# Optimization experiments

Measured on AMD Instinct MI355X. Metric: run time of the kernel, lower is better.

The kernel has to match this reference:

```python
import jax, jax.numpy as jnp
import numpy as np

V = 50000
E = 640000
DIM = 128
NUM_EDGE_TYPES = 32


def setup_inputs() -> dict:
    key = jax.random.key(0)
    ks = jax.random.split(key, 8)
    return {
        "node_values": jax.random.normal(ks[0], (V, DIM), dtype=jnp.float32),
        "edge_src": jax.random.randint(ks[1], (E,), 0, V, dtype=jnp.int32),
        "edge_dest": jax.random.randint(ks[2], (E,), 0, V, dtype=jnp.int32),
        "edge_cls": jax.random.randint(ks[3], (E,), 0, NUM_EDGE_TYPES, dtype=jnp.int32),
        "W_src": jax.random.normal(ks[4], (DIM, DIM), dtype=jnp.float32) / np.sqrt(DIM),
        "b_src": jnp.zeros((DIM,), dtype=jnp.float32),
        "W_dest": jax.random.normal(ks[5], (DIM, DIM), dtype=jnp.float32) / np.sqrt(DIM),
        "b_dest": jnp.zeros((DIM,), dtype=jnp.float32),
        "edge_emb": jax.random.normal(ks[6], (NUM_EDGE_TYPES, DIM), dtype=jnp.float32),
    }


def reference(node_values, edge_src, edge_dest, edge_cls, W_src, b_src, W_dest, b_dest, edge_emb):
    # Dense projections over all nodes, then gather per edge (matches tf.gather(dense(...), idx))
    src_proj = node_values @ W_src + b_src    # [V, dim]
    dest_proj = node_values @ W_dest + b_dest  # [V, dim]
    # Per-edge fused message: gather src, gather dest, edge-class embedding lookup, add, relu
    msgs = jax.nn.relu(src_proj[edge_src] + dest_proj[edge_dest] + edge_emb[edge_cls])  # [E, dim]
    # Scatter-reduce messages onto destination nodes
    out = jax.ops.segment_sum(msgs, edge_dest, num_segments=V)  # [V, dim]
    return out
```

## Files before the change

### kernel.cpp

```cpp
#include <hip/hip_runtime.h>


#define V 50000
#define E 640000
#define DIM 128
#define NXCD 8
#define DRANGE 6250
#define NBIN_R 50
#define BINW 125
#define BINCAP 2048
#define NCHUNK 256
#define EC4 625
#define QCAP 384

typedef __bf16 bf16x8 __attribute__((ext_vector_type(8)));
typedef float  f32x4  __attribute__((ext_vector_type(4)));
typedef float  f32x2  __attribute__((ext_vector_type(2)));

__device__ __forceinline__ float bf2f(unsigned int u16) {
    union { unsigned int i; float f; } c; c.i = u16 << 16; return c.f;
}
__device__ __forceinline__ unsigned int f2bf(float f) {
    union { float f; unsigned int i; } c; c.f = f;
    unsigned int u = c.i;
    return (u + 0x7FFFu + ((u >> 16) & 1u)) >> 16;
}

__global__ __launch_bounds__(256) void mp_binA(
    const int* __restrict__ ed, const int* __restrict__ es, const int* __restrict__ ec,
    const float* __restrict__ Ws, const float* __restrict__ Wd,
    const float* __restrict__ emb,
    unsigned short* __restrict__ Wpk, unsigned short* __restrict__ embB,
    int* __restrict__ binCnt, int* __restrict__ binbuf)
{
    __shared__ int hist[4][NBIN_R];
    __shared__ int cur[NBIN_R];
    const int r = blockIdx.x & (NXCD - 1);
    const int c = blockIdx.x >> 3;
    const int dlo = r * DRANGE;
    const int t = threadIdx.x;
    const int wv = t >> 6;

    if (blockIdx.x < 16) {
        int tid = blockIdx.x * 256 + t;
        int mat  = tid >> 11;
        int rem  = tid & 2047;
        int ct   = rem >> 8;
        int kt   = (rem >> 6) & 3;
        int lane = rem & 63;
        const float* W = mat ? Wd : Ws;
        int n  = ct * 16 + (lane & 15);
        int k0 = kt * 32 + (lane >> 4) * 8;
        unsigned short* dst = Wpk + (size_t)tid * 8;
        #pragma unroll
        for (int j = 0; j < 8; ++j) dst[j] = (unsigned short)f2bf(W[(k0 + j) * DIM + n]);
        embB[tid] = (unsigned short)f2bf(emb[tid]);
    }

    if (t < 4 * NBIN_R) ((int*)hist)[t] = 0;
    __syncthreads();

    int4 DV[3], SV[3], CV[3];
    {
        const int4* ed4 = (const int4*)ed + c * EC4;
        const int4* es4 = (const int4*)es + c * EC4;
        const int4* ec4 = (const int4*)ec + c * EC4;
        #pragma unroll
        for (int k = 0; k < 3; ++k) {
            int i = t + k * 256;
            if (i < EC4) { DV[k] = ed4[i]; SV[k] = es4[i]; CV[k] = ec4[i]; }
            else { DV[k] = make_int4(-1, -1, -1, -1);
                   SV[k] = make_int4(0, 0, 0, 0); CV[k] = make_int4(0, 0, 0, 0); }
        }
    }

    #pragma unroll
    for (int k = 0; k < 3; ++k) {
        int rel;
        rel = DV[k].x - dlo; if ((unsigned)rel < DRANGE) atomicAdd(&hist[wv][(unsigned)rel / BINW], 1);
        rel = DV[k].y - dlo; if ((unsigned)rel < DRANGE) atomicAdd(&hist[wv][(unsigned)rel / BINW], 1);
        rel = DV[k].z - dlo; if ((unsigned)rel < DRANGE) atomicAdd(&hist[wv][(unsigned)rel / BINW], 1);
        rel = DV[k].w - dlo; if ((unsigned)rel < DRANGE) atomicAdd(&hist[wv][(unsigned)rel / BINW], 1);
    }
    __syncthreads();

    if (t < NBIN_R) {
        int h = hist[0][t] + hist[1][t] + hist[2][t] + hist[3][t];
        cur[t] = atomicAdd(&binCnt[r * NBIN_R + t], h);
    }
    __syncthreads();

    #pragma unroll
    for (int k = 0; k < 3; ++k) {
        #define TRY(D, S, C) { \
            int rel = (D) - dlo; \
            if ((unsigned)rel < DRANGE) { \
                int bin = (unsigned)rel / BINW; \
                int rl  = rel - bin * BINW; \
                int pos = atomicAdd(&cur[bin], 1); \
                if ((unsigned)pos < BINCAP) \
                    binbuf[(r * NBIN_R + bin) * BINCAP + pos] = \
                        ((S) & 0xFFFF) | ((C) << 16) | (rl << 21); \
            } }
        TRY(DV[k].x, SV[k].x, CV[k].x); TRY(DV[k].y, SV[k].y, CV[k].y);
        TRY(DV[k].z, SV[k].z, CV[k].z); TRY(DV[k].w, SV[k].w, CV[k].w);
        #undef TRY
    }
}

__global__ __launch_bounds__(256) void mp_proj(
    const float* __restrict__ x, const unsigned short* __restrict__ Wpk,
    const float* __restrict__ bs, const float* __restrict__ bd,
    unsigned char* __restrict__ ps8, unsigned short* __restrict__ pdB)
{
    __shared__ float stage[4][16 * 132];
    const int wave = __builtin_amdgcn_readfirstlane(threadIdx.x) >> 6;
    const int lane = threadIdx.x & 63;
    const int m = lane & 15, q = lane >> 4;
    const int row0 = blockIdx.x * 64 + wave * 16;

    int arow = row0 + m; if (arow >= V) arow = V - 1;
    const float* xr = x + (size_t)arow * DIM + q * 8;

    bf16x8 A[4];
    #pragma unroll
    for (int kt = 0; kt < 4; ++kt) {
        float4 u = *(const float4*)(xr + kt * 32);
        float4 v = *(const float4*)(xr + kt * 32 + 4);
        bf16x8 a;
        a[0] = (__bf16)u.x; a[1] = (__bf16)u.y; a[2] = (__bf16)u.z; a[3] = (__bf16)u.w;
        a[4] = (__bf16)v.x; a[5] = (__bf16)v.y; a[6] = (__bf16)v.z; a[7] = (__bf16)v.w;
        A[kt] = a;
    }

    const bf16x8* Bp = (const bf16x8*)Wpk;

    f32x4 accS[8], accD[8];
    #pragma unroll
    for (int ct = 0; ct < 8; ++ct) {
        f32x4 aS = {0.f, 0.f, 0.f, 0.f}, aD = {0.f, 0.f, 0.f, 0.f};
        #pragma unroll
        for (int kt = 0; kt < 4; ++kt) {
            bf16x8 bS = Bp[((0 * 8 + ct) * 4 + kt) * 64 + lane];
            bf16x8 bD = Bp[((1 * 8 + ct) * 4 + kt) * 64 + lane];
            aS = __builtin_amdgcn_mfma_f32_16x16x32_bf16(A[kt], bS, aS, 0, 0, 0);
            aD = __builtin_amdgcn_mfma_f32_16x16x32_bf16(A[kt], bD, aD, 0, 0, 0);
        }
        accS[ct] = aS; accD[ct] = aD;
    }

    float* st = stage[wave];
    const int rr = lane & 15, cg = lane >> 4;
    const int orow = row0 + rr;
    const float* rowp = st + rr * 132 + cg * 32;

    #pragma unroll
    for (int ct = 0; ct < 8; ++ct) {
        const float bv = bs[ct * 16 + m];
        #pragma unroll
        for (int r = 0; r < 4; ++r)
            st[(q * 4 + r) * 132 + ct * 16 + m] = accS[ct][r] + bv;
    }
    __syncthreads();
    {
        int w[8];
        #pragma unroll
        for (int j = 0; j < 8; ++j) {
            float4 f = *(const float4*)(rowp + 4 * j);
            int v = __builtin_amdgcn_cvt_pk_fp8_f32(f.x, f.y, 0, false);
            v = __builtin_amdgcn_cvt_pk_fp8_f32(f.z, f.w, v, true);
            w[j] = v;
        }
        if (orow < V) {
            int4* dst = (int4*)(ps8 + (size_t)orow * 128 + cg * 32);
            dst[0] = make_int4(w[0], w[1], w[2], w[3]);
            dst[1] = make_int4(w[4], w[5], w[6], w[7]);
        }
    }
    __syncthreads();

    #pragma unroll
    for (int ct = 0; ct < 8; ++ct) {
        const float bv = bd[ct * 16 + m];
        #pragma unroll
        for (int r = 0; r < 4; ++r)
            st[(q * 4 + r) * 132 + ct * 16 + m] = accD[ct][r] + bv;
    }
    __syncthreads();
    {
        int w[16];
        #pragma unroll
        for (int j = 0; j < 8; ++j) {
            float4 f = *(const float4*)(rowp + 4 * j);
            w[2 * j]     = f2bf(f.x) | (f2bf(f.y) << 16);
            w[2 * j + 1] = f2bf(f.z) | (f2bf(f.w) << 16);
        }
        if (orow < V) {
            int4* dst = (int4*)(pdB + (size_t)orow * 128 + cg * 32);
            #pragma unroll
            for (int jj = 0; jj < 4; ++jj)
                dst[jj] = make_int4(w[4 * jj], w[4 * jj + 1], w[4 * jj + 2], w[4 * jj + 3]);
        }
    }
}

__global__ __launch_bounds__(256) void mp_binBC(
    const unsigned char* __restrict__ ps8, const unsigned short* __restrict__ pdB,
    const unsigned short* __restrict__ embB,
    const int* __restrict__ binCnt, const int* __restrict__ binbuf,
    float* __restrict__ out)
{
    __shared__ int csr[QCAP];
    __shared__ int cnt[16];
    __shared__ int off[17];
    __shared__ int cur[16];

    const int r = blockIdx.x & (NXCD - 1);
    const int rest = blockIdx.x >> 3;
    const int bi = rest % NBIN_R;
    const int qu = rest / NBIN_R;
    const int bin = r * NBIN_R + bi;
    const int rel0 = qu * 16;
    const int relW = (qu == 7) ? 13 : 16;
    const int d0 = bin * BINW + rel0;
    const int t = threadIdx.x;

    int nb = binCnt[bin]; if (nb > BINCAP) nb = BINCAP;
    const int* buf = binbuf + (size_t)bin * BINCAP;

    if (t < 16) cnt[t] = 0;
    __syncthreads();

    int EB[8];
    #pragma unroll
    for (int k = 0; k < 8; ++k) {
        int i = t + k * 256;
        EB[k] = (i < nb) ? buf[i] : -1;
    }

    #pragma unroll
    for (int k = 0; k < 8; ++k) {
        int rl = (int)((unsigned)EB[k] >> 21) - rel0;
        if ((unsigned)rl < (unsigned)relW) atomicAdd(&cnt[rl], 1);
    }
    __syncthreads();

    if (t < 16) {
        int v = (t < relW) ? cnt[t] : 0;
        #pragma unroll
        for (int dlt = 1; dlt < 16; dlt <<= 1) {
            int u = __shfl_up(v, dlt, 64);
            if (t >= dlt) v += u;
        }
        off[t + 1] = v;
        cur[t] = v - cnt[t];
        if (t == 0) off[0] = 0;
    }
    __syncthreads();

    #pragma unroll
    for (int k = 0; k < 8; ++k) {
        int rl = (int)((unsigned)EB[k] >> 21) - rel0;
        if ((unsigned)rl < (unsigned)relW) {
            int pos = atomicAdd(&cur[rl], 1);
            if (pos < QCAP) csr[pos] = EB[k];
        }
    }
    __syncthreads();

    const int wave = t >> 6, lane = t & 63;
    #define PROC(P) { \
        int s_ = *(const unsigned short*)(ps8 + ((size_t)((P) & 0xFFFF) << 7) + 2 * lane); \
        unsigned int e_ = *(const unsigned int*)(embB + ((((P) >> 16) & 0x1F) << 7) + 2 * lane); \
        f32x2 f_ = __builtin_amdgcn_cvt_pk_f32_fp8(s_, false); \
        a0 += fmaxf(f_.x + dp0 + bf2f(e_ & 0xFFFF), 0.f); \
        a1 += fmaxf(f_.y + dp1 + bf2f(e_ >> 16),    0.f); }

    for (int rl = wave; rl < relW; rl += 4) {
        const int d = d0 + rl;
        int i0 = off[rl], i1 = off[rl + 1];
        if (i1 > QCAP) i1 = QCAP;
        if (i0 > i1) i0 = i1;
        unsigned int pdu = *(const unsigned int*)(pdB + (size_t)d * DIM + 2 * lane);
        const float dp0 = bf2f(pdu & 0xFFFF), dp1 = bf2f(pdu >> 16);
        float a0 = 0.f, a1 = 0.f;
        int i = i0;
        for (; i + 8 <= i1; i += 8) {
            int p0 = csr[i],     p1 = csr[i + 1], p2 = csr[i + 2], p3 = csr[i + 3];
            int p4 = csr[i + 4], p5 = csr[i + 5], p6 = csr[i + 6], p7 = csr[i + 7];
            PROC(p0); PROC(p1); PROC(p2); PROC(p3);
            PROC(p4); PROC(p5); PROC(p6); PROC(p7);
        }
        for (; i + 4 <= i1; i += 4) {
            int p0 = csr[i], p1 = csr[i + 1], p2 = csr[i + 2], p3 = csr[i + 3];
            PROC(p0); PROC(p1); PROC(p2); PROC(p3);
        }
        for (; i < i1; ++i) { int p0 = csr[i]; PROC(p0); }
        *(float2*)(out + (size_t)d * DIM + 2 * lane) = make_float2(a0, a1);
    }
    #undef PROC
}

extern "C" void kernel_launch(void* const* d_in, const int* in_sizes, int n_in,
                              void* d_out, int out_size, void* d_ws, size_t ws_size,
                              hipStream_t stream) {
    const float* x   = (const float*)d_in[0];
    const int*   es  = (const int*)d_in[1];
    const int*   ed  = (const int*)d_in[2];
    const int*   ec  = (const int*)d_in[3];
    const float* Ws  = (const float*)d_in[4];
    const float* bs  = (const float*)d_in[5];
    const float* Wd  = (const float*)d_in[6];
    const float* bd  = (const float*)d_in[7];
    const float* emb = (const float*)d_in[8];
    float* out = (float*)d_out;

    char* ws = (char*)d_ws;
    size_t off = 0;
    unsigned char*  ps8  = (unsigned char*)(ws + off);  off += (size_t)V * 128;
    unsigned short* pdB  = (unsigned short*)(ws + off); off += (size_t)V * DIM * 2;
    int* binbuf = (int*)(ws + off);                     off += (size_t)400 * BINCAP * 4;
    int* binCnt = (int*)(ws + off);                     off += 400 * 4;
    unsigned short* Wpk  = (unsigned short*)(ws + off); off += 2 * 128 * 128 * 2;
    unsigned short* embB = (unsigned short*)(ws + off); off += 32 * 128 * 2;

    hipMemsetAsync(binCnt, 0, 400 * 4, stream);
    mp_binA<<<NXCD * NCHUNK, 256, 0, stream>>>(ed, es, ec, Ws, Wd, emb, Wpk, embB, binCnt, binbuf);
    mp_proj<<<(V + 63) / 64, 256, 0, stream>>>(x, Wpk, bs, bd, ps8, pdB);
    mp_binBC<<<NBIN_R * NXCD * 8, 256, 0, stream>>>(ps8, pdB, embB, binCnt, binbuf, out);
}
```

Baseline: 154.7 us.

## Use 16-node bins so each consumer block reads only its own bin

Changes the destination binning from 50 bins of 125 nodes per XCD to 391 bins of 16 nodes, using shift and mask in place of division. Each consumer block now loads only its own small bin (up to 320 entries) instead of scanning a 2048-entry bin and discarding seven eighths of it, which removes redundant global reads and filtering. The destination projection rows are also prefetched before the first barrier. The cost is a larger shared histogram and more global bin counters and atomics in the binning kernel, and the per-bin capacity of 320 could overflow on skewed inputs.

```diff
diff --git a/kernel.cpp b/kernel.cpp
--- a/kernel.cpp
+++ b/kernel.cpp
@@ -6,12 +6,10 @@
 #define DIM 128
 #define NXCD 8
 #define DRANGE 6250
-#define NBIN_R 50
-#define BINW 125
-#define BINCAP 2048
+#define NBIN_R 391
+#define BINCAP 320
 #define NCHUNK 256
 #define EC4 625
-#define QCAP 384
 
 typedef __bf16 bf16x8 __attribute__((ext_vector_type(8)));
 typedef float  f32x4  __attribute__((ext_vector_type(4)));
@@ -57,7 +55,7 @@
         embB[tid] = (unsigned short)f2bf(emb[tid]);
     }
 
-    if (t < 4 * NBIN_R) ((int*)hist)[t] = 0;
+    for (int i = t; i < 4 * NBIN_R; i += 256) ((int*)hist)[i] = 0;
     __syncthreads();
 
     int4 DV[3], SV[3], CV[3];
@@ -77,16 +75,16 @@
     #pragma unroll
     for (int k = 0; k < 3; ++k) {
         int rel;
-        rel = DV[k].x - dlo; if ((unsigned)rel < DRANGE) atomicAdd(&hist[wv][(unsigned)rel / BINW], 1);
-        rel = DV[k].y - dlo; if ((unsigned)rel < DRANGE) atomicAdd(&hist[wv][(unsigned)rel / BINW], 1);
-        rel = DV[k].z - dlo; if ((unsigned)rel < DRANGE) atomicAdd(&hist[wv][(unsigned)rel / BINW], 1);
-        rel = DV[k].w - dlo; if ((unsigned)rel < DRANGE) atomicAdd(&hist[wv][(unsigned)rel / BINW], 1);
-    }
-    __syncthreads();
-
-    if (t < NBIN_R) {
-        int h = hist[0][t] + hist[1][t] + hist[2][t] + hist[3][t];
-        cur[t] = atomicAdd(&binCnt[r * NBIN_R + t], h);
+        rel = DV[k].x - dlo; if ((unsigned)rel < DRANGE) atomicAdd(&hist[wv][(unsigned)rel >> 4], 1);
+        rel = DV[k].y - dlo; if ((unsigned)rel < DRANGE) atomicAdd(&hist[wv][(unsigned)rel >> 4], 1);
+        rel = DV[k].z - dlo; if ((unsigned)rel < DRANGE) atomicAdd(&hist[wv][(unsigned)rel >> 4], 1);
+        rel = DV[k].w - dlo; if ((unsigned)rel < DRANGE) atomicAdd(&hist[wv][(unsigned)rel >> 4], 1);
+    }
+    __syncthreads();
+
+    for (int i = t; i < NBIN_R; i += 256) {
+        int h = hist[0][i] + hist[1][i] + hist[2][i] + hist[3][i];
+        cur[i] = atomicAdd(&binCnt[r * NBIN_R + i], h);
     }
     __syncthreads();
 
@@ -95,8 +93,8 @@
         #define TRY(D, S, C) { \
             int rel = (D) - dlo; \
             if ((unsigned)rel < DRANGE) { \
-                int bin = (unsigned)rel / BINW; \
-                int rl  = rel - bin * BINW; \
+                int bin = (unsigned)rel >> 4; \
+                int rl  = rel & 15; \
                 int pos = atomicAdd(&cur[bin], 1); \
                 if ((unsigned)pos < BINCAP) \
                     binbuf[(r * NBIN_R + bin) * BINCAP + pos] = \
@@ -210,38 +208,43 @@
     const int* __restrict__ binCnt, const int* __restrict__ binbuf,
     float* __restrict__ out)
 {
-    __shared__ int csr[QCAP];
+    __shared__ int csr[BINCAP];
     __shared__ int cnt[16];
     __shared__ int off[17];
     __shared__ int cur[16];
 
     const int r = blockIdx.x & (NXCD - 1);
-    const int rest = blockIdx.x >> 3;
-    const int bi = rest % NBIN_R;
-    const int qu = rest / NBIN_R;
-    const int bin = r * NBIN_R + bi;
-    const int rel0 = qu * 16;
-    const int relW = (qu == 7) ? 13 : 16;
-    const int d0 = bin * BINW + rel0;
+    const int g = blockIdx.x >> 3;
+    const int bin = r * NBIN_R + g;
+    const int rel0 = g * 16;
+    const int relW = (rel0 + 16 <= DRANGE) ? 16 : (DRANGE - rel0);
+    const int d0 = r * DRANGE + rel0;
     const int t = threadIdx.x;
+    const int wave = t >> 6, lane = t & 63;
 
     int nb = binCnt[bin]; if (nb > BINCAP) nb = BINCAP;
     const int* buf = binbuf + (size_t)bin * BINCAP;
 
     if (t < 16) cnt[t] = 0;
-    __syncthreads();
-
-    int EB[8];
-    #pragma unroll
-    for (int k = 0; k < 8; ++k) {
-        int i = t + k * 256;
-        EB[k] = (i < nb) ? buf[i] : -1;
-    }
-
-    #pragma unroll
-    for (int k = 0; k < 8; ++k) {
-        int rl = (int)((unsigned)EB[k] >> 21) - rel0;
-        if ((unsigned)rl < (unsigned)relW) atomicAdd(&cnt[rl], 1);
+
+    int EB[2];
+    EB[0] = (t < nb) ? buf[t] : -1;
+    EB[1] = (t + 256 < nb) ? buf[t + 256] : -1;
+
+    float dp0v[4], dp1v[4];
+    #pragma unroll
+    for (int k = 0; k < 4; ++k) {
+        int rl = wave + k * 4;
+        int d = d0 + ((rl < relW) ? rl : 0);
+        unsigned int pdu = *(const unsigned int*)(pdB + (size_t)d * DIM + 2 * lane);
+        dp0v[k] = bf2f(pdu & 0xFFFF); dp1v[k] = bf2f(pdu >> 16);
+    }
+    __syncthreads();
+
+    #pragma unroll
+    for (int k = 0; k < 2; ++k) {
+        int rl = (int)((unsigned)EB[k] >> 21);
+        if (EB[k] != -1) atomicAdd(&cnt[rl], 1);
     }
     __syncthreads();
 
@@ -259,16 +262,15 @@
     __syncthreads();
 
     #pragma unroll
-    for (int k = 0; k < 8; ++k) {
-        int rl = (int)((unsigned)EB[k] >> 21) - rel0;
-        if ((unsigned)rl < (unsigned)relW) {
+    for (int k = 0; k < 2; ++k) {
+        if (EB[k] != -1) {
+            int rl = (int)((unsigned)EB[k] >> 21);
             int pos = atomicAdd(&cur[rl], 1);
-            if (pos < QCAP) csr[pos] = EB[k];
-        }
-    }
-    __syncthreads();
-
-    const int wave = t >> 6, lane = t & 63;
+            csr[pos] = EB[k];
+        }
+    }
+    __syncthreads();
+
     #define PROC(P) { \
         int s_ = *(const unsigned short*)(ps8 + ((size_t)((P) & 0xFFFF) << 7) + 2 * lane); \
         unsigned int e_ = *(const unsigned int*)(embB + ((((P) >> 16) & 0x1F) << 7) + 2 * lane); \
@@ -276,13 +278,13 @@
         a0 += fmaxf(f_.x + dp0 + bf2f(e_ & 0xFFFF), 0.f); \
         a1 += fmaxf(f_.y + dp1 + bf2f(e_ >> 16),    0.f); }
 
-    for (int rl = wave; rl < relW; rl += 4) {
+    #pragma unroll
+    for (int k = 0; k < 4; ++k) {
+        const int rl = wave + k * 4;
+        if (rl >= relW) break;
         const int d = d0 + rl;
         int i0 = off[rl], i1 = off[rl + 1];
-        if (i1 > QCAP) i1 = QCAP;
-        if (i0 > i1) i0 = i1;
-        unsigned int pdu = *(const unsigned int*)(pdB + (size_t)d * DIM + 2 * lane);
-        const float dp0 = bf2f(pdu & 0xFFFF), dp1 = bf2f(pdu >> 16);
+        const float dp0 = dp0v[k], dp1 = dp1v[k];
         float a0 = 0.f, a1 = 0.f;
         int i = i0;
         for (; i + 8 <= i1; i += 8) {
@@ -319,13 +321,13 @@
     size_t off = 0;
     unsigned char*  ps8  = (unsigned char*)(ws + off);  off += (size_t)V * 128;
     unsigned short* pdB  = (unsigned short*)(ws + off); off += (size_t)V * DIM * 2;
-    int* binbuf = (int*)(ws + off);                     off += (size_t)400 * BINCAP * 4;
-    int* binCnt = (int*)(ws + off);                     off += 400 * 4;
+    int* binbuf = (int*)(ws + off);                     off += (size_t)NXCD * NBIN_R * BINCAP * 4;
+    int* binCnt = (int*)(ws + off);                     off += (size_t)NXCD * NBIN_R * 4;
     unsigned short* Wpk  = (unsigned short*)(ws + off); off += 2 * 128 * 128 * 2;
     unsigned short* embB = (unsigned short*)(ws + off); off += 32 * 128 * 2;
 
-    hipMemsetAsync(binCnt, 0, 400 * 4, stream);
+    hipMemsetAsync(binCnt, 0, (size_t)NXCD * NBIN_R * 4, stream);
     mp_binA<<<NXCD * NCHUNK, 256, 0, stream>>>(ed, es, ec, Ws, Wd, emb, Wpk, embB, binCnt, binbuf);
     mp_proj<<<(V + 63) / 64, 256, 0, stream>>>(x, Wpk, bs, bd, ps8, pdB);
-    mp_binBC<<<NBIN_R * NXCD * 8, 256, 0, stream>>>(ps8, pdB, embB, binCnt, binbuf, out);
-}
+    mp_binBC<<<NXCD * NBIN_R, 256, 0, stream>>>(ps8, pdB, embB, binCnt, binbuf, out);
+}
```

New measurement: 156.4 us. No clear change (+1.1%).

## Locally sort edges by bin in LDS before coalesced binbuf writes; prefetch dest projections

Applied to the files above, without the earlier changes.

The binning kernel now stages each chunk's in-range edges in shared memory, prefix-sums a per-bin histogram, and sorts the edges by bin locally. Each bin's edges are then written to global binbuf as contiguous runs instead of scattered per-edge atomic-slot writes, which should improve write coalescing. The gather kernel issues its dest-projection loads early, before the counting sync, so their latency overlaps with the CSR build. In exchange the binning kernel uses more shared memory and more barriers, and edges beyond NE_MAX per block are dropped silently.

```diff
diff --git a/kernel.cpp b/kernel.cpp
--- a/kernel.cpp
+++ b/kernel.cpp
@@ -11,6 +11,7 @@
 #define BINCAP 2048
 #define NCHUNK 256
 #define EC4 625
+#define NE_MAX 512
 #define QCAP 384
 
 typedef __bf16 bf16x8 __attribute__((ext_vector_type(8)));
@@ -33,13 +34,20 @@
     unsigned short* __restrict__ Wpk, unsigned short* __restrict__ embB,
     int* __restrict__ binCnt, int* __restrict__ binbuf)
 {
-    __shared__ int hist[4][NBIN_R];
-    __shared__ int cur[NBIN_R];
+    __shared__ int ebuf[NE_MAX];
+    __shared__ unsigned char bbin[NE_MAX];
+    __shared__ int csr[NE_MAX];
+    __shared__ unsigned char sbin[NE_MAX];
+    __shared__ int hist[NBIN_R];
+    __shared__ int lofs[NBIN_R + 1];
+    __shared__ int lcur[NBIN_R];
+    __shared__ int gbase[NBIN_R];
+    __shared__ int ecnt;
+
     const int r = blockIdx.x & (NXCD - 1);
     const int c = blockIdx.x >> 3;
     const int dlo = r * DRANGE;
     const int t = threadIdx.x;
-    const int wv = t >> 6;
 
     if (blockIdx.x < 16) {
         int tid = blockIdx.x * 256 + t;
@@ -57,7 +65,8 @@
         embB[tid] = (unsigned short)f2bf(emb[tid]);
     }
 
-    if (t < 4 * NBIN_R) ((int*)hist)[t] = 0;
+    if (t < NBIN_R) hist[t] = 0;
+    if (t == 0) ecnt = 0;
     __syncthreads();
 
     int4 DV[3], SV[3], CV[3];
@@ -76,35 +85,51 @@
 
     #pragma unroll
     for (int k = 0; k < 3; ++k) {
-        int rel;
-        rel = DV[k].x - dlo; if ((unsigned)rel < DRANGE) atomicAdd(&hist[wv][(unsigned)rel / BINW], 1);
-        rel = DV[k].y - dlo; if ((unsigned)rel < DRANGE) atomicAdd(&hist[wv][(unsigned)rel / BINW], 1);
-        rel = DV[k].z - dlo; if ((unsigned)rel < DRANGE) atomicAdd(&hist[wv][(unsigned)rel / BINW], 1);
-        rel = DV[k].w - dlo; if ((unsigned)rel < DRANGE) atomicAdd(&hist[wv][(unsigned)rel / BINW], 1);
-    }
-    __syncthreads();
-
-    if (t < NBIN_R) {
-        int h = hist[0][t] + hist[1][t] + hist[2][t] + hist[3][t];
-        cur[t] = atomicAdd(&binCnt[r * NBIN_R + t], h);
-    }
-    __syncthreads();
-
-    #pragma unroll
-    for (int k = 0; k < 3; ++k) {
-        #define TRY(D, S, C) { \
+        #define PUSH(D, S, C) { \
             int rel = (D) - dlo; \
             if ((unsigned)rel < DRANGE) { \
                 int bin = (unsigned)rel / BINW; \
                 int rl  = rel - bin * BINW; \
-                int pos = atomicAdd(&cur[bin], 1); \
-                if ((unsigned)pos < BINCAP) \
-                    binbuf[(r * NBIN_R + bin) * BINCAP + pos] = \
-                        ((S) & 0xFFFF) | ((C) << 16) | (rl << 21); \
-            } }
-        TRY(DV[k].x, SV[k].x, CV[k].x); TRY(DV[k].y, SV[k].y, CV[k].y);
-        TRY(DV[k].z, SV[k].z, CV[k].z); TRY(DV[k].w, SV[k].w, CV[k].w);
-        #undef TRY
+                atomicAdd(&hist[bin], 1); \
+                int pos = atomicAdd(&ecnt, 1); \
+                if (pos < NE_MAX) { \
+                    ebuf[pos] = ((S) & 0xFFFF) | ((C) << 16) | (rl << 21); \
+                    bbin[pos] = (unsigned char)bin; \
+                } } }
+        PUSH(DV[k].x, SV[k].x, CV[k].x); PUSH(DV[k].y, SV[k].y, CV[k].y);
+        PUSH(DV[k].z, SV[k].z, CV[k].z); PUSH(DV[k].w, SV[k].w, CV[k].w);
+        #undef PUSH
+    }
+    __syncthreads();
+
+    if (t < NBIN_R) gbase[t] = atomicAdd(&binCnt[r * NBIN_R + t], hist[t]);
+    if (t < 64) {
+        int v = (t < NBIN_R) ? hist[t] : 0;
+        #pragma unroll
+        for (int dlt = 1; dlt < 64; dlt <<= 1) {
+            int u = __shfl_up(v, dlt, 64);
+            if (t >= dlt) v += u;
+        }
+        if (t < NBIN_R) { lofs[t + 1] = v; lcur[t] = v - hist[t]; }
+        if (t == 0) lofs[0] = 0;
+    }
+    __syncthreads();
+
+    int ne = ecnt; if (ne > NE_MAX) ne = NE_MAX;
+
+    for (int i = t; i < ne; i += 256) {
+        int b = bbin[i];
+        int p = atomicAdd(&lcur[b], 1);
+        csr[p] = ebuf[i];
+        sbin[p] = (unsigned char)b;
+    }
+    __syncthreads();
+
+    for (int i = t; i < ne; i += 256) {
+        int b = sbin[i];
+        int slot = gbase[b] + (i - lofs[b]);
+        if (slot < BINCAP)
+            binbuf[(r * NBIN_R + b) * BINCAP + slot] = csr[i];
     }
 }
 
@@ -224,12 +249,12 @@
     const int relW = (qu == 7) ? 13 : 16;
     const int d0 = bin * BINW + rel0;
     const int t = threadIdx.x;
+    const int wave = t >> 6, lane = t & 63;
 
     int nb = binCnt[bin]; if (nb > BINCAP) nb = BINCAP;
     const int* buf = binbuf + (size_t)bin * BINCAP;
 
     if (t < 16) cnt[t] = 0;
-    __syncthreads();
 
     int EB[8];
     #pragma unroll
@@ -237,6 +262,16 @@
         int i = t + k * 256;
         EB[k] = (i < nb) ? buf[i] : -1;
     }
+
+    float dp0v[4], dp1v[4];
+    #pragma unroll
+    for (int k = 0; k < 4; ++k) {
+        int rl = wave + k * 4;
+        int d = d0 + ((rl < relW) ? rl : 0);
+        unsigned int pdu = *(const unsigned int*)(pdB + (size_t)d * DIM + 2 * lane);
+        dp0v[k] = bf2f(pdu & 0xFFFF); dp1v[k] = bf2f(pdu >> 16);
+    }
+    __syncthreads();
 
     #pragma unroll
     for (int k = 0; k < 8; ++k) {
@@ -268,7 +303,6 @@
     }
     __syncthreads();
 
-    const int wave = t >> 6, lane = t & 63;
     #define PROC(P) { \
         int s_ = *(const unsigned short*)(ps8 + ((size_t)((P) & 0xFFFF) << 7) + 2 * lane); \
         unsigned int e_ = *(const unsigned int*)(embB + ((((P) >> 16) & 0x1F) << 7) + 2 * lane); \
@@ -276,13 +310,15 @@
         a0 += fmaxf(f_.x + dp0 + bf2f(e_ & 0xFFFF), 0.f); \
         a1 += fmaxf(f_.y + dp1 + bf2f(e_ >> 16),    0.f); }
 
-    for (int rl = wave; rl < relW; rl += 4) {
+    #pragma unroll
+    for (int k = 0; k < 4; ++k) {
+        const int rl = wave + k * 4;
+        if (rl >= relW) break;
         const int d = d0 + rl;
         int i0 = off[rl], i1 = off[rl + 1];
         if (i1 > QCAP) i1 = QCAP;
         if (i0 > i1) i0 = i1;
-        unsigned int pdu = *(const unsigned int*)(pdB + (size_t)d * DIM + 2 * lane);
-        const float dp0 = bf2f(pdu & 0xFFFF), dp1 = bf2f(pdu >> 16);
+        const float dp0 = dp0v[k], dp1 = dp1v[k];
         float a0 = 0.f, a1 = 0.f;
         int i = i0;
         for (; i + 8 <= i1; i += 8) {
```

Measured after the change: 154.3 us. About the same (-0.2%).
